# Performance work log

Measured on AMD Instinct MI355X. Metric: run time of the kernel, lower is better.

The kernel has to match this reference:

```python
import jax, jax.numpy as jnp
import numpy as np

# Chambolle-Pock / Condat over-relaxed primal-dual constants (from _TVDenoiser.__init__)
TAU = 0.01
RHO = 1.99
SIGMA = 1.0 / TAU / 8.0  # 1/tau/8, 8 = Lipschitz const of D^T D in 2D
THS = 0.1                # lambda (denoise threshold)
NITER = 40
CRIT = 1e-5


def nabla2(x):
    """Forward finite differences: x (..., H, W) -> u (..., H, W, 2).
    Channel 0: diff along H (rows), channel 1: diff along W (cols); last
    row/col of each channel is zero (as in the deepinv original)."""
    dh = jnp.zeros_like(x).at[..., :-1, :].set(x[..., 1:, :] - x[..., :-1, :])
    dw = jnp.zeros_like(x).at[..., :, :-1].set(x[..., :, 1:] - x[..., :, :-1])
    return jnp.stack([dh, dw], axis=-1)


def nabla2_adjoint(u):
    """Adjoint of nabla2: u (..., H, W, 2) -> (..., H, W)."""
    v0 = u[..., :-1, :, 0]  # (..., H-1, W)
    v1 = u[..., :, :-1, 1]  # (..., H, W-1)
    out = jnp.zeros(u.shape[:-1], u.dtype)
    out = out.at[..., :-1, :].add(-v0).at[..., 1:, :].add(v0)
    out = out.at[..., :, :-1].add(-v1).at[..., :, 1:].add(v1)
    return out


def _step(x2, u2, y):
    # prox_tau_fx: (x + tau*y)/(1+tau)
    x = (x2 - TAU * nabla2_adjoint(u2) + TAU * y) / (1.0 + TAU)
    # prox_sigma_g_conj: project gradient field onto L2 ball of radius lambda
    v = u2 + SIGMA * nabla2(2.0 * x - x2)
    mag = jnp.sqrt(jnp.sum(v * v, axis=-1))  # (..., H, W)
    u = v / jnp.maximum(mag / THS, 1.0)[..., None]
    # over-relaxation
    x2n = x2 + RHO * (x - x2)
    u2n = u2 + RHO * (u - u2)
    return x2n, u2n


def setup_inputs() -> dict:
    key = jax.random.key(0)
    y = jax.random.normal(key, (8, 512, 512), dtype=jnp.float32)
    return {"y": y}


def reference(y):
    # warm restart init: x2 = y, u2 = 0 (restart branch of forward)
    u0 = jnp.zeros(y.shape + (2,), y.dtype)

    def cond(state):
        x2, u2, it, rel = state
        # original breaks at end of iteration _ if _ > 1 and rel_err < crit
        return (it < NITER) & jnp.logical_not((it >= 3) & (rel < CRIT))

    def body(state):
        x2, u2, it, _ = state
        x2n, u2n = _step(x2, u2, y)
        rel = jnp.linalg.norm((x2 - x2n).ravel()) / jnp.linalg.norm(
            x2n.ravel() + 1e-12
        )
        return (x2n, u2n, it + 1, rel)

    x2, u2, it, rel = jax.lax.while_loop(
        cond, body, (y, u0, jnp.int32(0), jnp.float32(jnp.inf))
    )
    return x2
```

## Files before the change

### kernel.cpp

```cpp
#include <hip/hip_runtime.h>


#define Hh 512
#define Ww 512
#define Bb 8
#define TSC 112
#define TSR 48
#define KF 8
#define SC 128
#define SR 64
#define NT 512
#define RS 8

__global__ __launch_bounds__(NT, 2)
void tv_packed(const float*  __restrict__ y_in,
               const float4* __restrict__ st_in,
               float4* __restrict__ st_out,
               float*  __restrict__ x2_out,
               int first, int last)
{
    constexpr float TAU = 0.01f;
    constexpr float RHO = 1.99f;
    constexpr float HRHO = 0.995f;
    constexpr float SIGMA = 12.5f;
    constexpr float THS = 0.1f;
    constexpr float INV_1PT = 1.0f / 1.01f;

    __shared__ float u0B [9 * SC];
    __shared__ float wTop[9 * SC];

    const int b   = blockIdx.z;
    const int r0  = blockIdx.y * TSR;
    const int c0  = blockIdx.x * TSC;
    const int tid = threadIdx.x;
    const size_t plane = (size_t)b * (Hh * Ww);

    const int s     = tid >> 6;
    const int lc    = tid & 63;
    const int lcol0 = 2 * lc;
    const int gc0   = c0 - KF + lcol0;
    const bool colin0 = (gc0 >= 0) & (gc0 < Ww);
    const bool colin1 = (gc0 + 1 >= 0) & (gc0 + 1 < Ww);
    const float sewf0 = (gc0     < Ww - 1) ? SIGMA : 0.f;
    const float sewf1 = (gc0 + 1 < Ww - 1) ? SIGMA : 0.f;
    const int lr0 = RS * s;
    const int gr0 = r0 - KF + lr0;
    const float sigBot = (gr0 + RS - 1 == Hh - 1) ? 0.f : SIGMA;

    if (tid < SC) { u0B[tid] = 0.f; wTop[8 * SC + tid] = 0.f; }

    float x2[RS][2], u0[RS][2], u1[RS][2], yv[RS][2], w[RS][2];
    unsigned tmp[4] = {0u, 0u, 0u, 0u};

    #pragma unroll
    for (int i = 0; i < RS; ++i) {
        const int gr = gr0 + i;
        const int lr = lr0 + i;
        const bool rin = (gr >= 0) & (gr < Hh);
        #pragma unroll
        for (int c = 0; c < 2; ++c) {
            const bool img = rin & (c ? colin1 : colin0);
            const size_t gi = img ? (plane + (size_t)gr * Ww + (gc0 + c)) : plane;
            if (first) {
                float cy = y_in[gi]; cy = img ? cy : 0.f;
                x2[i][c] = cy; yv[i][c] = cy; u0[i][c] = 0.f; u1[i][c] = 0.f;
            } else {
                float4 st = st_in[gi];
                x2[i][c] = img ? st.x : 0.f;
                u0[i][c] = img ? st.y : 0.f;
                u1[i][c] = img ? st.z : 0.f;
                yv[i][c] = img ? st.w : 0.f;
            }
            const int lcol = lcol0 + c;
            unsigned tm = img ? (unsigned)min(min(lr, SR - 1 - lr),
                                              min(lcol, SC - 1 - lcol)) : 0u;
            const int k = 2 * i + c;
            tmp[k >> 2] |= tm << (8 * (k & 3));
        }
    }
    *(float2*)&u0B[(s + 1) * SC + lcol0] = make_float2(u0[RS - 1][0], u0[RS - 1][1]);
    __syncthreads();

    for (int t = 0; t < KF; ++t) {
        {
            float2 ua2 = *(float2*)&u0B[s * SC + lcol0];
            #pragma unroll
            for (int i = 0; i < RS; ++i) {
                float ul0 = __shfl_up(u1[i][1], 1, 64);
                float ul1 = u1[i][0];
                float ua_0 = (i == 0) ? ua2.x : u0[i - 1][0];
                float ua_1 = (i == 0) ? ua2.y : u0[i - 1][1];
                float adj0 = ua_0 - u0[i][0] + ul0 - u1[i][0];
                float adj1 = ua_1 - u0[i][1] + ul1 - u1[i][1];
                float xv0 = fmaf(TAU, yv[i][0] - adj0, x2[i][0]);
                float xv1 = fmaf(TAU, yv[i][1] - adj1, x2[i][1]);
                w[i][0] = fmaf(2.0f * INV_1PT, xv0, -x2[i][0]);
                w[i][1] = fmaf(2.0f * INV_1PT, xv1, -x2[i][1]);
            }
            *(float2*)&wTop[s * SC + lcol0] = make_float2(w[0][0], w[0][1]);
        }
        __syncthreads();
        {
            float2 wb2 = *(float2*)&wTop[(s + 1) * SC + lcol0];
            #pragma unroll
            for (int i = 0; i < RS; ++i) {
                float wr1 = __shfl_down(w[i][0], 1, 64);
                float wr0 = w[i][1];
                float wb_0 = (i == RS - 1) ? wb2.x : w[i + 1][0];
                float wb_1 = (i == RS - 1) ? wb2.y : w[i + 1][1];
                const float sig_h = (i == RS - 1) ? sigBot : SIGMA;

                float v00 = fmaf(sig_h, wb_0 - w[i][0], u0[i][0]);
                float v10 = fmaf(sewf0, wr0 - w[i][0], u1[i][0]);
                float iv0 = fminf(THS * __builtin_amdgcn_rsqf(fmaf(v00, v00, v10 * v10)), 1.f);
                float v01 = fmaf(sig_h, wb_1 - w[i][1], u0[i][1]);
                float v11 = fmaf(sewf1, wr1 - w[i][1], u1[i][1]);
                float iv1 = fminf(THS * __builtin_amdgcn_rsqf(fmaf(v01, v01, v11 * v11)), 1.f);

                const int k0 = 2 * i, k1 = 2 * i + 1;
                unsigned tm0 = (tmp[k0 >> 2] >> (8 * (k0 & 3))) & 255u;
                unsigned tm1 = (tmp[k1 >> 2] >> (8 * (k1 & 3))) & 255u;
                bool a0 = (unsigned)t < tm0;
                bool a1 = (unsigned)t < tm1;
                float r10 = a0 ? RHO : 0.f, rh0 = a0 ? HRHO : 0.f;
                float r11 = a1 ? RHO : 0.f, rh1 = a1 ? HRHO : 0.f;

                u0[i][0] = fmaf(r10, fmaf(v00, iv0, -u0[i][0]), u0[i][0]);
                u1[i][0] = fmaf(r10, fmaf(v10, iv0, -u1[i][0]), u1[i][0]);
                x2[i][0] = fmaf(rh0, w[i][0] - x2[i][0], x2[i][0]);
                u0[i][1] = fmaf(r11, fmaf(v01, iv1, -u0[i][1]), u0[i][1]);
                u1[i][1] = fmaf(r11, fmaf(v11, iv1, -u1[i][1]), u1[i][1]);
                x2[i][1] = fmaf(rh1, w[i][1] - x2[i][1], x2[i][1]);
            }
            *(float2*)&u0B[(s + 1) * SC + lcol0] = make_float2(u0[RS - 1][0], u0[RS - 1][1]);
        }
        __syncthreads();
    }

    if (s >= 1 && s <= 6) {
        #pragma unroll
        for (int c = 0; c < 2; ++c) {
            const int lcol = lcol0 + c;
            const int gc   = gc0 + c;
            if (lcol >= KF && lcol < KF + TSC && gc < Ww) {
                #pragma unroll
                for (int i = 0; i < RS; ++i) {
                    const int gr = gr0 + i;
                    if (gr < Hh) {
                        const size_t gi = plane + (size_t)gr * Ww + gc;
                        if (last) x2_out[gi] = x2[i][c];
                        else      st_out[gi] = make_float4(x2[i][c], u0[i][c],
                                                           u1[i][c], yv[i][c]);
                    }
                }
            }
        }
    }
}

#define TS 48
#define S  64

__global__ __launch_bounds__(NT, 3)
void tv_sep(const float*  __restrict__ x2_in,
            const float2* __restrict__ u_in,
            const float*  __restrict__ y_in,
            float*  __restrict__ x2_out,
            float2* __restrict__ u_out,
            int first, int last)
{
    constexpr float TAU = 0.01f;
    constexpr float RHO = 1.99f;
    constexpr float HRHO = 0.995f;
    constexpr float SIGMA = 12.5f;
    constexpr float THS = 0.1f;
    constexpr float INV_1PT = 1.0f / 1.01f;

    __shared__ float u0B [9 * S];
    __shared__ float wTop[9 * S];

    const int b   = blockIdx.z;
    const int r0  = blockIdx.y * TS;
    const int c0  = blockIdx.x * TS;
    const int tid = threadIdx.x;
    const size_t plane = (size_t)b * (Hh * Ww);

    const int s   = tid >> 6;
    const int lc  = tid & 63;
    const int gc  = c0 - KF + lc;
    const bool colin = (gc >= 0) & (gc < Ww);
    const float sewf = (gc < Ww - 1) ? SIGMA : 0.f;
    const int lr0 = RS * s;
    const int gr0 = r0 - KF + lr0;
    const float sigBot = (gr0 + RS - 1 == Hh - 1) ? 0.f : SIGMA;

    if (tid < S) { u0B[tid] = 0.f; wTop[8 * S + tid] = 0.f; }

    float u0[RS], u1[RS], x2[RS], yv[RS], w[RS];
    unsigned tmp0 = 0u, tmp1 = 0u;

    #pragma unroll
    for (int i = 0; i < RS; ++i) {
        const int gr = gr0 + i;
        const int lr = lr0 + i;
        const bool img = colin & (gr >= 0) & (gr < Hh);
        float a = 0.f, c = 0.f, z0 = 0.f, z1 = 0.f;
        if (img) {
            size_t gi = plane + (size_t)gr * Ww + gc;
            c = y_in[gi];
            if (first) a = c;
            else {
                a = x2_in[gi];
                float2 uu = u_in[gi];
                z0 = uu.x; z1 = uu.y;
            }
        }
        u0[i] = z0; u1[i] = z1; x2[i] = a; yv[i] = c;
        unsigned tm = img ? (unsigned)min(min(lr, S - 1 - lr), min(lc, S - 1 - lc)) : 0u;
        if (i < 4) tmp0 |= tm << (8 * i);
        else       tmp1 |= tm << (8 * (i - 4));
    }
    u0B[(s + 1) * S + lc] = u0[RS - 1];
    __syncthreads();

    for (int t = 0; t < KF; ++t) {
        {
            float u0a = u0B[s * S + lc];
            #pragma unroll
            for (int i = 0; i < RS; ++i) {
                float ul = __shfl_up(u1[i], 1, 64);
                float ua = (i == 0) ? u0a : u0[i - 1];
                float adj = ua - u0[i] + ul - u1[i];
                float xv = fmaf(TAU, yv[i] - adj, x2[i]);
                w[i] = fmaf(2.0f * INV_1PT, xv, -x2[i]);
            }
            wTop[s * S + lc] = w[0];
        }
        __syncthreads();
        {
            float wbot = wTop[(s + 1) * S + lc];
            #pragma unroll
            for (int i = 0; i < RS; ++i) {
                float wr = __shfl_down(w[i], 1, 64);
                float wb = (i == RS - 1) ? wbot : w[i + 1];
                const float sig_h = (i == RS - 1) ? sigBot : SIGMA;
                float v0 = fmaf(sig_h, wb - w[i], u0[i]);
                float v1 = fmaf(sewf,  wr - w[i], u1[i]);
                float iv = fminf(THS * __builtin_amdgcn_rsqf(fmaf(v0, v0, v1 * v1)), 1.f);
                unsigned tmb = ((i < 4 ? tmp0 : tmp1) >> (8 * (i & 3))) & 255u;
                bool act = (unsigned)t < tmb;
                float r1 = act ? RHO  : 0.f;
                float rh = act ? HRHO : 0.f;
                u0[i] = fmaf(r1, fmaf(v0, iv, -u0[i]), u0[i]);
                u1[i] = fmaf(r1, fmaf(v1, iv, -u1[i]), u1[i]);
                x2[i] = fmaf(rh, w[i] - x2[i], x2[i]);
            }
            u0B[(s + 1) * S + lc] = u0[RS - 1];
        }
        __syncthreads();
    }

    if (s >= 1 && s <= 6 && lc >= KF && lc < KF + TS && gc < Ww) {
        #pragma unroll
        for (int i = 0; i < RS; ++i) {
            const int gr = gr0 + i;
            if (gr < Hh) {
                size_t gi = plane + (size_t)gr * Ww + gc;
                x2_out[gi] = x2[i];
                if (!last) u_out[gi] = make_float2(u0[i], u1[i]);
            }
        }
    }
}

extern "C" void kernel_launch(void* const* d_in, const int* in_sizes, int n_in,
                              void* d_out, int out_size, void* d_ws, size_t ws_size,
                              hipStream_t stream)
{
    const float* y = (const float*)d_in[0];
    float* out = (float*)d_out;
    const size_t NP = (size_t)Bb * Hh * Ww;

    if (ws_size >= 2 * NP * sizeof(float4)) {
        float4* stA = (float4*)d_ws;
        float4* stB = stA + NP;
        dim3 grid((Ww + TSC - 1) / TSC, (Hh + TSR - 1) / TSR, Bb);
        tv_packed<<<grid, NT, 0, stream>>>(y, stB, stA, out, 1, 0);
        tv_packed<<<grid, NT, 0, stream>>>(y, stA, stB, out, 0, 0);
        tv_packed<<<grid, NT, 0, stream>>>(y, stB, stA, out, 0, 0);
        tv_packed<<<grid, NT, 0, stream>>>(y, stA, stB, out, 0, 0);
        tv_packed<<<grid, NT, 0, stream>>>(y, stB, stA, out, 0, 1);
    } else {
        float*  ws  = (float*)d_ws;
        float*  x2A = ws;
        float*  x2B = ws + NP;
        float2* uA  = (float2*)(ws + 2 * NP);
        float2* uB  = (float2*)(ws + 4 * NP);
        dim3 grid((Ww + TS - 1) / TS, (Hh + TS - 1) / TS, Bb);
        tv_sep<<<grid, NT, 0, stream>>>(y,   uB, y, x2A, uA, 1, 0);
        tv_sep<<<grid, NT, 0, stream>>>(x2A, uA, y, x2B, uB, 0, 0);
        tv_sep<<<grid, NT, 0, stream>>>(x2B, uB, y, x2A, uA, 0, 0);
        tv_sep<<<grid, NT, 0, stream>>>(x2A, uA, y, x2B, uB, 0, 0);
        tv_sep<<<grid, NT, 0, stream>>>(x2B, uB, y, out, uA, 0, 1);
    }
}
```

Measured before the change: 222.6 us.

## Fuse ten iterations per launch with wider halo and add interior fast path

Raises the number of fused time steps per temporal-blocked launch from 8 to 10 by widening the halo and shrinking the output tile to 108x44. This cuts the chain from five launches to four, which removes one full state read/write round trip through global memory. It also adds a fast path for interior waves that skips per-element mask unpacking and uses a per-row sigma. In exchange, more halo cells are recomputed per tile and there are more tiles in the grid; correctness depends on the 10-step halo staying inside the 64-row, 128-column buffer.

```diff
diff --git a/kernel.cpp b/kernel.cpp
--- a/kernel.cpp
+++ b/kernel.cpp
@@ -4,9 +4,9 @@
 #define Hh 512
 #define Ww 512
 #define Bb 8
-#define TSC 112
-#define TSR 48
-#define KF 8
+#define KF 10
+#define TSC 108
+#define TSR 44
 #define SC 128
 #define SR 64
 #define NT 512
@@ -45,11 +45,15 @@
     const float sewf1 = (gc0 + 1 < Ww - 1) ? SIGMA : 0.f;
     const int lr0 = RS * s;
     const int gr0 = r0 - KF + lr0;
-    const float sigBot = (gr0 + RS - 1 == Hh - 1) ? 0.f : SIGMA;
+
+    const int colTm0 = colin0 ? min(lcol0,     SC - 1 - lcol0) : 0;
+    const int colTm1 = colin1 ? min(lcol0 + 1, SC - 2 - lcol0) : 0;
+    const bool midwave = (s >= 2) & (s <= 5) & (gr0 >= 0) & (gr0 + RS - 1 < Hh);
 
     if (tid < SC) { u0B[tid] = 0.f; wTop[8 * SC + tid] = 0.f; }
 
     float x2[RS][2], u0[RS][2], u1[RS][2], yv[RS][2], w[RS][2];
+    float sigH[RS];
     unsigned tmp[4] = {0u, 0u, 0u, 0u};
 
     #pragma unroll
@@ -57,6 +61,7 @@
         const int gr = gr0 + i;
         const int lr = lr0 + i;
         const bool rin = (gr >= 0) & (gr < Hh);
+        sigH[i] = (gr == Hh - 1) ? 0.f : SIGMA;
         #pragma unroll
         for (int c = 0; c < 2; ++c) {
             const bool img = rin & (c ? colin1 : colin0);
@@ -102,56 +107,77 @@
         __syncthreads();
         {
             float2 wb2 = *(float2*)&wTop[(s + 1) * SC + lcol0];
+            if (midwave) {
+                const bool a0 = t < colTm0;
+                const bool a1 = t < colTm1;
+                const float r10 = a0 ? RHO : 0.f, rh0 = a0 ? HRHO : 0.f;
+                const float r11 = a1 ? RHO : 0.f, rh1 = a1 ? HRHO : 0.f;
+                #pragma unroll
+                for (int i = 0; i < RS; ++i) {
+                    float wr1 = __shfl_down(w[i][0], 1, 64);
+                    float wr0 = w[i][1];
+                    float wb_0 = (i == RS - 1) ? wb2.x : w[i + 1][0];
+                    float wb_1 = (i == RS - 1) ? wb2.y : w[i + 1][1];
+                    float v00 = fmaf(sigH[i], wb_0 - w[i][0], u0[i][0]);
+                    float v10 = fmaf(sewf0,   wr0 - w[i][0], u1[i][0]);
+                    float iv0 = fminf(THS * __builtin_amdgcn_rsqf(fmaf(v00, v00, v10 * v10)), 1.f);
+                    float v01 = fmaf(sigH[i], wb_1 - w[i][1], u0[i][1]);
+                    float v11 = fmaf(sewf1,   wr1 - w[i][1], u1[i][1]);
+                    float iv1 = fminf(THS * __builtin_amdgcn_rsqf(fmaf(v01, v01, v11 * v11)), 1.f);
+                    u0[i][0] = fmaf(r10, fmaf(v00, iv0, -u0[i][0]), u0[i][0]);
+                    u1[i][0] = fmaf(r10, fmaf(v10, iv0, -u1[i][0]), u1[i][0]);
+                    x2[i][0] = fmaf(rh0, w[i][0] - x2[i][0], x2[i][0]);
+                    u0[i][1] = fmaf(r11, fmaf(v01, iv1, -u0[i][1]), u0[i][1]);
+                    u1[i][1] = fmaf(r11, fmaf(v11, iv1, -u1[i][1]), u1[i][1]);
+                    x2[i][1] = fmaf(rh1, w[i][1] - x2[i][1], x2[i][1]);
+                }
+            } else {
+                #pragma unroll
+                for (int i = 0; i < RS; ++i) {
+                    float wr1 = __shfl_down(w[i][0], 1, 64);
+                    float wr0 = w[i][1];
+                    float wb_0 = (i == RS - 1) ? wb2.x : w[i + 1][0];
+                    float wb_1 = (i == RS - 1) ? wb2.y : w[i + 1][1];
+                    float v00 = fmaf(sigH[i], wb_0 - w[i][0], u0[i][0]);
+                    float v10 = fmaf(sewf0,   wr0 - w[i][0], u1[i][0]);
+                    float iv0 = fminf(THS * __builtin_amdgcn_rsqf(fmaf(v00, v00, v10 * v10)), 1.f);
+                    float v01 = fmaf(sigH[i], wb_1 - w[i][1], u0[i][1]);
+                    float v11 = fmaf(sewf1,   wr1 - w[i][1], u1[i][1]);
+                    float iv1 = fminf(THS * __builtin_amdgcn_rsqf(fmaf(v01, v01, v11 * v11)), 1.f);
+                    const int k0 = 2 * i, k1 = 2 * i + 1;
+                    unsigned tm0 = (tmp[k0 >> 2] >> (8 * (k0 & 3))) & 255u;
+                    unsigned tm1 = (tmp[k1 >> 2] >> (8 * (k1 & 3))) & 255u;
+                    bool a0 = (unsigned)t < tm0;
+                    bool a1 = (unsigned)t < tm1;
+                    float r10 = a0 ? RHO : 0.f, rh0 = a0 ? HRHO : 0.f;
+                    float r11 = a1 ? RHO : 0.f, rh1 = a1 ? HRHO : 0.f;
+                    u0[i][0] = fmaf(r10, fmaf(v00, iv0, -u0[i][0]), u0[i][0]);
+                    u1[i][0] = fmaf(r10, fmaf(v10, iv0, -u1[i][0]), u1[i][0]);
+                    x2[i][0] = fmaf(rh0, w[i][0] - x2[i][0], x2[i][0]);
+                    u0[i][1] = fmaf(r11, fmaf(v01, iv1, -u0[i][1]), u0[i][1]);
+                    u1[i][1] = fmaf(r11, fmaf(v11, iv1, -u1[i][1]), u1[i][1]);
+                    x2[i][1] = fmaf(rh1, w[i][1] - x2[i][1], x2[i][1]);
+                }
+            }
+            *(float2*)&u0B[(s + 1) * SC + lcol0] = make_float2(u0[RS - 1][0], u0[RS - 1][1]);
+        }
+        __syncthreads();
+    }
+
+    #pragma unroll
+    for (int c = 0; c < 2; ++c) {
+        const int lcol = lcol0 + c;
+        const int gc   = gc0 + c;
+        if (lcol >= KF && lcol < KF + TSC && gc < Ww) {
             #pragma unroll
             for (int i = 0; i < RS; ++i) {
-                float wr1 = __shfl_down(w[i][0], 1, 64);
-                float wr0 = w[i][1];
-                float wb_0 = (i == RS - 1) ? wb2.x : w[i + 1][0];
-                float wb_1 = (i == RS - 1) ? wb2.y : w[i + 1][1];
-                const float sig_h = (i == RS - 1) ? sigBot : SIGMA;
-
-                float v00 = fmaf(sig_h, wb_0 - w[i][0], u0[i][0]);
-                float v10 = fmaf(sewf0, wr0 - w[i][0], u1[i][0]);
-                float iv0 = fminf(THS * __builtin_amdgcn_rsqf(fmaf(v00, v00, v10 * v10)), 1.f);
-                float v01 = fmaf(sig_h, wb_1 - w[i][1], u0[i][1]);
-                float v11 = fmaf(sewf1, wr1 - w[i][1], u1[i][1]);
-                float iv1 = fminf(THS * __builtin_amdgcn_rsqf(fmaf(v01, v01, v11 * v11)), 1.f);
-
-                const int k0 = 2 * i, k1 = 2 * i + 1;
-                unsigned tm0 = (tmp[k0 >> 2] >> (8 * (k0 & 3))) & 255u;
-                unsigned tm1 = (tmp[k1 >> 2] >> (8 * (k1 & 3))) & 255u;
-                bool a0 = (unsigned)t < tm0;
-                bool a1 = (unsigned)t < tm1;
-                float r10 = a0 ? RHO : 0.f, rh0 = a0 ? HRHO : 0.f;
-                float r11 = a1 ? RHO : 0.f, rh1 = a1 ? HRHO : 0.f;
-
-                u0[i][0] = fmaf(r10, fmaf(v00, iv0, -u0[i][0]), u0[i][0]);
-                u1[i][0] = fmaf(r10, fmaf(v10, iv0, -u1[i][0]), u1[i][0]);
-                x2[i][0] = fmaf(rh0, w[i][0] - x2[i][0], x2[i][0]);
-                u0[i][1] = fmaf(r11, fmaf(v01, iv1, -u0[i][1]), u0[i][1]);
-                u1[i][1] = fmaf(r11, fmaf(v11, iv1, -u1[i][1]), u1[i][1]);
-                x2[i][1] = fmaf(rh1, w[i][1] - x2[i][1], x2[i][1]);
-            }
-            *(float2*)&u0B[(s + 1) * SC + lcol0] = make_float2(u0[RS - 1][0], u0[RS - 1][1]);
-        }
-        __syncthreads();
-    }
-
-    if (s >= 1 && s <= 6) {
-        #pragma unroll
-        for (int c = 0; c < 2; ++c) {
-            const int lcol = lcol0 + c;
-            const int gc   = gc0 + c;
-            if (lcol >= KF && lcol < KF + TSC && gc < Ww) {
-                #pragma unroll
-                for (int i = 0; i < RS; ++i) {
-                    const int gr = gr0 + i;
-                    if (gr < Hh) {
-                        const size_t gi = plane + (size_t)gr * Ww + gc;
-                        if (last) x2_out[gi] = x2[i][c];
-                        else      st_out[gi] = make_float4(x2[i][c], u0[i][c],
-                                                           u1[i][c], yv[i][c]);
-                    }
+                const int lr = lr0 + i;
+                const int gr = gr0 + i;
+                if (lr >= KF && lr < KF + TSR && gr < Hh) {
+                    const size_t gi = plane + (size_t)gr * Ww + gc;
+                    if (last) x2_out[gi] = x2[i][c];
+                    else      st_out[gi] = make_float4(x2[i][c], u0[i][c],
+                                                       u1[i][c], yv[i][c]);
                 }
             }
         }
@@ -160,6 +186,7 @@
 
 #define TS 48
 #define S  64
+#define FK 8
 
 __global__ __launch_bounds__(NT, 3)
 void tv_sep(const float*  __restrict__ x2_in,
@@ -187,11 +214,11 @@
 
     const int s   = tid >> 6;
     const int lc  = tid & 63;
-    const int gc  = c0 - KF + lc;
+    const int gc  = c0 - FK + lc;
     const bool colin = (gc >= 0) & (gc < Ww);
     const float sewf = (gc < Ww - 1) ? SIGMA : 0.f;
     const int lr0 = RS * s;
-    const int gr0 = r0 - KF + lr0;
+    const int gr0 = r0 - FK + lr0;
     const float sigBot = (gr0 + RS - 1 == Hh - 1) ? 0.f : SIGMA;
 
     if (tid < S) { u0B[tid] = 0.f; wTop[8 * S + tid] = 0.f; }
@@ -223,7 +250,7 @@
     u0B[(s + 1) * S + lc] = u0[RS - 1];
     __syncthreads();
 
-    for (int t = 0; t < KF; ++t) {
+    for (int t = 0; t < FK; ++t) {
         {
             float u0a = u0B[s * S + lc];
             #pragma unroll
@@ -260,7 +287,7 @@
         __syncthreads();
     }
 
-    if (s >= 1 && s <= 6 && lc >= KF && lc < KF + TS && gc < Ww) {
+    if (s >= 1 && s <= 6 && lc >= FK && lc < FK + TS && gc < Ww) {
         #pragma unroll
         for (int i = 0; i < RS; ++i) {
             const int gr = gr0 + i;
@@ -288,8 +315,7 @@
         tv_packed<<<grid, NT, 0, stream>>>(y, stB, stA, out, 1, 0);
         tv_packed<<<grid, NT, 0, stream>>>(y, stA, stB, out, 0, 0);
         tv_packed<<<grid, NT, 0, stream>>>(y, stB, stA, out, 0, 0);
-        tv_packed<<<grid, NT, 0, stream>>>(y, stA, stB, out, 0, 0);
-        tv_packed<<<grid, NT, 0, stream>>>(y, stB, stA, out, 0, 1);
+        tv_packed<<<grid, NT, 0, stream>>>(y, stA, stB, out, 0, 1);
     } else {
         float*  ws  = (float*)d_ws;
         float*  x2A = ws;
```

New measurement: 239.2 us. +7.5%, slower.
